# Performance work log

Hardware: AMD Instinct MI355X
Metric: run time of the kernel (lower is better)

## Reference

```python
import jax, jax.numpy as jnp
import numpy as np
import math

N_NODES = 100000
N_GRAPHS = 8
EDGES_PER_GRAPH = 200000
F = 128
RATIO = 0.8


def setup_inputs() -> dict:
    key = jax.random.key(0)
    ks = jax.random.split(key, 24)
    n = N_NODES // N_GRAPHS
    x = jax.random.normal(ks[0], (N_NODES, F), jnp.float32)
    # block-diagonal edges: each graph's edges stay within its node range
    offs = (jnp.arange(N_GRAPHS, dtype=jnp.int32) * n)[:, None]
    src = jax.random.randint(ks[1], (N_GRAPHS, EDGES_PER_GRAPH), 0, n, jnp.int32) + offs
    dst = jax.random.randint(ks[2], (N_GRAPHS, EDGES_PER_GRAPH), 0, n, jnp.int32) + offs
    edge_index = jnp.stack([src.reshape(-1), dst.reshape(-1)])

    def lin(k, fi, fo):
        return jax.random.normal(k, (fo, fi), jnp.float32) / np.sqrt(fi).astype(np.float32)

    inp = dict(x=x, edge_index=edge_index)
    for i, k0 in zip((1, 2, 3), (3, 8, 13)):
        inp[f"W{i}_lin"] = lin(ks[k0], F, F)
        inp[f"b{i}_lin"] = jnp.zeros((F,), jnp.float32)
        inp[f"W{i}_upd"] = lin(ks[k0 + 1], 2 * F, F)   # no bias in update_lin
        inp[f"wp{i}"] = jax.random.normal(ks[k0 + 2], (F,), jnp.float32) / np.float32(np.sqrt(F))
    inp["Wl1"] = lin(ks[18], 2 * F, F); inp["bl1"] = jnp.zeros((F,), jnp.float32)
    inp["Wl2"] = lin(ks[19], F, 64);    inp["bl2"] = jnp.zeros((64,), jnp.float32)
    inp["Wl3"] = lin(ks[20], 64, 1);    inp["bl3"] = jnp.zeros((1,), jnp.float32)
    inp["num_graphs"] = N_GRAPHS
    return inp


def sage_conv(x, edges, W_lin, b_lin, W_upd):
    """Custom SAGEConv: add self loops, msg = relu(lin(x_j)), scatter-max,
    update = relu(update_lin(cat([aggr, x]))). Dummy node at index M absorbs
    edges to/from dropped nodes (never fed back to real nodes)."""
    M = x.shape[0]
    x_ext = jnp.concatenate([x, jnp.zeros((1, x.shape[1]), x.dtype)], 0)  # [M+1, F]
    loops = jnp.arange(M + 1, dtype=edges.dtype)
    src = jnp.concatenate([edges[0], loops])
    dst = jnp.concatenate([edges[1], loops])
    msg = jax.nn.relu(x_ext[src] @ W_lin.T + b_lin)            # gather + linear + relu  [E+M+1, F]
    aggr = jax.ops.segment_max(msg, dst, num_segments=M + 1)   # scatter-max (self loops -> no empty seg)
    out = jax.nn.relu(jnp.concatenate([aggr, x_ext], -1) @ W_upd.T)
    return out[:M]


def topk_pool(x, edges, w, B):
    """TopKPooling(ratio=0.8): score = x.w/||w||, keep top-k per graph,
    x' = x[perm] * tanh(score[perm]); edges remapped, dropped -> dummy Mn."""
    M = x.shape[0]
    n = M // B
    k = int(math.ceil(RATIO * n))
    Mn = B * k
    s = (x @ w) / jnp.linalg.norm(w)
    vals, idx = jax.lax.top_k(s.reshape(B, n), k)              # [B, k]
    gidx = (idx + (jnp.arange(B, dtype=idx.dtype) * n)[:, None]).reshape(-1)
    x_new = x[gidx] * jnp.tanh(vals).reshape(-1)[:, None]
    newpos = jnp.full((M + 1,), Mn, dtype=edges.dtype).at[gidx].set(
        jnp.arange(Mn, dtype=edges.dtype))
    e = newpos[edges]
    invalid = (e[0] == Mn) | (e[1] == Mn)
    e = jnp.where(invalid[None, :], Mn, e)                     # route dropped edges to dummy
    return x_new, e


def readout(x, B):
    xb = x.reshape(B, -1, x.shape[1])                          # graphs are equal-sized
    return jnp.concatenate([xb.max(1), xb.mean(1)], -1)        # gmp || gap  [B, 2F]


def reference(x, edge_index, W1_lin, b1_lin, W1_upd, wp1, W2_lin, b2_lin, W2_upd, wp2,
              W3_lin, b3_lin, W3_upd, wp3, Wl1, bl1, Wl2, bl2, Wl3, bl3, num_graphs):
    B = num_graphs
    h = jax.nn.relu(sage_conv(x, edge_index, W1_lin, b1_lin, W1_upd))
    h, e = topk_pool(h, edge_index, wp1, B); x1 = readout(h, B)
    h = jax.nn.relu(sage_conv(h, e, W2_lin, b2_lin, W2_upd))
    h, e = topk_pool(h, e, wp2, B);          x2 = readout(h, B)
    h = jax.nn.relu(sage_conv(h, e, W3_lin, b3_lin, W3_upd))
    h, e = topk_pool(h, e, wp3, B);          x3 = readout(h, B)
    z = x1 + x2 + x3
    z = jax.nn.relu(z @ Wl1.T + bl1)
    z = jax.nn.relu(z @ Wl2.T + bl2)
    # dropout is identity in eval mode
    return jax.nn.sigmoid(z @ Wl3.T + bl3)[:, 0]
```

## Files before the change

kernel.cpp:

```cpp
#include <hip/hip_runtime.h>
#include <math.h>


typedef unsigned int uint;
typedef unsigned long long ull;

typedef _Float16 h8v __attribute__((ext_vector_type(8)));
typedef _Float16 h4v __attribute__((ext_vector_type(4)));
typedef _Float16 h2v __attribute__((ext_vector_type(2)));
typedef float v4f __attribute__((ext_vector_type(4)));

struct hl16 { _Float16 hi, lo; };

__device__ __forceinline__ float4 ld4(const float* p) { return *reinterpret_cast<const float4*>(p); }
__device__ __forceinline__ float2 ld2(const float* p) { return *reinterpret_cast<const float2*>(p); }

__device__ __forceinline__ uint mono32(float f) {
    uint b = __float_as_uint(f);
    return b ^ ((uint)((int)b >> 31) | 0x80000000u);
}

__device__ __forceinline__ hl16 split16(float x) {
    hl16 r;
    r.hi = (_Float16)x;
    r.lo = (_Float16)(x - (float)r.hi);
    return r;
}

__device__ __forceinline__ h8v hmax8(h8v a, h8v b) {
    return __builtin_elementwise_max(a, b);
}

template<int K, bool A0Z, bool OUT16>
__global__ __launch_bounds__(256, 2)
void mfma_gemm(const _Float16* __restrict__ A0hi, const _Float16* __restrict__ A0lo,
               const _Float16* __restrict__ A1hi, const _Float16* __restrict__ A1lo,
               const _Float16* __restrict__ Whi, const _Float16* __restrict__ Wlo,
               const float* __restrict__ bias, void* __restrict__ outv, int M)
{
    constexpr int LDT = 40;
    __shared__ __align__(16) _Float16 As[128 * LDT];
    __shared__ __align__(16) _Float16 Ws[128 * LDT];
    const int tid = threadIdx.x;
    const int lane = tid & 63;
    const int wv = tid >> 6;
    const int wr = (wv >> 1) * 64;
    const int wc = (wv & 1) * 64;
    const int quad = lane >> 4;
    const int l16 = lane & 15;
    const int row0 = blockIdx.x * 128;

    const int sr0 = tid >> 2;
    const int sr1 = sr0 + 64;
    const int sq = (tid & 3) * 8;
    const bool ok0 = (row0 + sr0) < M;
    const bool ok1 = (row0 + sr1) < M;

    v4f acc[4][4];
#pragma unroll
    for (int i = 0; i < 4; ++i)
#pragma unroll
        for (int j = 0; j < 4; ++j) acc[i][j] = (v4f){0.f, 0.f, 0.f, 0.f};

    constexpr int CPS = K / 32;
    constexpr int NS2 = A0Z ? (K - 128) / 32 : CPS;
    constexpr int NC = 2 * CPS + NS2;
    float4 pa0, pa1, pw0, pw1;
    const float4 f4z = make_float4(0.f, 0.f, 0.f, 0.f);

#define GLOAD(C) do { \
        int kc_, kk_; const _Float16 *Wp_, *Ap_; bool lo_ = (C) >= 2 * CPS; \
        if ((C) < CPS)          { kc_ = (C) * 32;          Wp_ = Whi; } \
        else if ((C) < 2 * CPS) { kc_ = ((C) - CPS) * 32;  Wp_ = Wlo; } \
        else                    { kc_ = ((C) - 2 * CPS) * 32 + (A0Z ? 128 : 0); Wp_ = Whi; } \
        if (K == 256 && kc_ >= 128) { Ap_ = lo_ ? A1lo : A1hi; kk_ = kc_ - 128; } \
        else                        { Ap_ = lo_ ? A0lo : A0hi; kk_ = kc_; } \
        pa0 = ok0 ? ld4((const float*)(Ap_ + (size_t)(row0 + sr0) * 128 + kk_ + sq)) : f4z; \
        pa1 = ok1 ? ld4((const float*)(Ap_ + (size_t)(row0 + sr1) * 128 + kk_ + sq)) : f4z; \
        pw0 = ld4((const float*)(Wp_ + (size_t)sr0 * K + kc_ + sq)); \
        pw1 = ld4((const float*)(Wp_ + (size_t)sr1 * K + kc_ + sq)); \
    } while (0)

#define SSTORE() do { \
        *reinterpret_cast<float4*>(&As[sr0 * LDT + sq]) = pa0; \
        *reinterpret_cast<float4*>(&As[sr1 * LDT + sq]) = pa1; \
        *reinterpret_cast<float4*>(&Ws[sr0 * LDT + sq]) = pw0; \
        *reinterpret_cast<float4*>(&Ws[sr1 * LDT + sq]) = pw1; \
    } while (0)

    GLOAD(0);
#pragma unroll
    for (int c = 0; c < NC; ++c) {
        SSTORE();
        __syncthreads();
        if (c + 1 < NC) GLOAD(c + 1);
        h8v af[4], bf[4];
#pragma unroll
        for (int rt = 0; rt < 4; ++rt)
            af[rt] = *reinterpret_cast<const h8v*>(&As[(wr + rt * 16 + l16) * LDT + quad * 8]);
#pragma unroll
        for (int ct = 0; ct < 4; ++ct)
            bf[ct] = *reinterpret_cast<const h8v*>(&Ws[(wc + ct * 16 + l16) * LDT + quad * 8]);
#pragma unroll
        for (int rt = 0; rt < 4; ++rt)
#pragma unroll
            for (int ct = 0; ct < 4; ++ct)
                acc[rt][ct] = __builtin_amdgcn_mfma_f32_16x16x32_f16(
                    af[rt], bf[ct], acc[rt][ct], 0, 0, 0);
        if (c + 1 < NC) __syncthreads();
    }
#undef GLOAD
#undef SSTORE

    float bv[4];
#pragma unroll
    for (int ct = 0; ct < 4; ++ct)
        bv[ct] = bias ? bias[wc + ct * 16 + l16] : 0.f;
#pragma unroll
    for (int rt = 0; rt < 4; ++rt) {
        int rb = row0 + wr + rt * 16 + quad * 4;
#pragma unroll
        for (int r = 0; r < 4; ++r) {
            int row = rb + r;
            if (row < M) {
                if (OUT16) {
                    _Float16* op = (_Float16*)outv + (size_t)row * 128;
#pragma unroll
                    for (int ct = 0; ct < 4; ++ct)
                        op[wc + ct * 16 + l16] =
                            (_Float16)fmaxf(acc[rt][ct][r] + bv[ct], 0.f);
                } else {
                    float* op = (float*)outv + (size_t)row * 128;
#pragma unroll
                    for (int ct = 0; ct < 4; ++ct)
                        op[wc + ct * 16 + l16] = fmaxf(acc[rt][ct][r] + bv[ct], 0.f);
                }
            }
        }
    }
}

__global__ void prep_weights(const float* __restrict__ s0, const float* __restrict__ s1,
                             const float* __restrict__ s2, const float* __restrict__ s3,
                             const float* __restrict__ s4, const float* __restrict__ s5,
                             _Float16* __restrict__ WLhi, _Float16* __restrict__ WLlo,
                             _Float16* __restrict__ WUhi, _Float16* __restrict__ WUlo)
{
    int i = blockIdx.x * 256 + threadIdx.x;
    if (i < 3 * 16384) {
        int m = i / 16384, o = i - m * 16384;
        const float* s = (m == 0) ? s0 : (m == 1) ? s2 : s4;
        hl16 r = split16(s[o]);
        WLhi[i] = r.hi; WLlo[i] = r.lo;
    } else if (i < 3 * 16384 + 3 * 32768) {
        int j = i - 3 * 16384;
        int m = j / 32768, o = j - m * 32768;
        const float* s = (m == 0) ? s1 : (m == 1) ? s3 : s5;
        hl16 r = split16(s[o]);
        WUhi[j] = r.hi; WUlo[j] = r.lo;
    }
}

__global__ void convert_x(const float* __restrict__ x, _Float16* __restrict__ hi,
                          _Float16* __restrict__ lo, int total4)
{
    int i = blockIdx.x * 256 + threadIdx.x;
    if (i >= total4) return;
    float4 v = ld4(x + (size_t)i * 4);
    h4v H, L;
    hl16 r0 = split16(v.x); H[0] = r0.hi; L[0] = r0.lo;
    hl16 r1 = split16(v.y); H[1] = r1.hi; L[1] = r1.lo;
    hl16 r2 = split16(v.z); H[2] = r2.hi; L[2] = r2.lo;
    hl16 r3 = split16(v.w); H[3] = r3.hi; L[3] = r3.lo;
    *reinterpret_cast<h4v*>(hi + (size_t)i * 4) = H;
    *reinterpret_cast<h4v*>(lo + (size_t)i * 4) = L;
}

#define SC_T 16
#define SC_CH (256 * SC_T)
__global__ __launch_bounds__(256)
void bucket_scatter(const int* __restrict__ esrc, const int* __restrict__ edst,
                    int* __restrict__ bcur, uint* __restrict__ bkt,
                    int Eg, int n, int NB, int CAP)
{
    __shared__ int lcnt[64];
    __shared__ int lbase[64];
    int g = blockIdx.x & 7;
    int c = blockIdx.x >> 3;
    int t = threadIdx.x;
    if (t < 64) lcnt[t] = 0;
    __syncthreads();
    int e0i = c * SC_CH;
    uint pk[SC_T];
    int bkid[SC_T];
    int loc[SC_T];
#pragma unroll
    for (int j = 0; j < SC_T; ++j) {
        int o = e0i + j * 256 + t;
        bkid[j] = -1;
        if (o < Eg) {
            int i = g * Eg + o;
            int dl = edst[i] - g * n;
            int b = dl >> 8;
            pk[j] = ((uint)dl << 17) | (uint)esrc[i];
            bkid[j] = b;
            loc[j] = atomicAdd(&lcnt[b], 1);
        }
    }
    __syncthreads();
    if (t < NB && lcnt[t] > 0)
        lbase[t] = atomicAdd(&bcur[g * NB + t], lcnt[t]);
    __syncthreads();
#pragma unroll
    for (int j = 0; j < SC_T; ++j) {
        if (bkid[j] >= 0) {
            int b = bkid[j];
            int slot = lbase[b] + loc[j];
            if (slot < CAP)
                bkt[(size_t)(g * NB + b) * CAP + slot] = pk[j];
        }
    }
}

__global__ __launch_bounds__(256)
void csr_build(const int* __restrict__ bcur, const uint* __restrict__ bkt,
               int* __restrict__ rowptr, int* __restrict__ csr,
               int Eg, int n, int NB, int CAP)
{
    __shared__ uint eLDS[5120];
    __shared__ int outLDS[5120];
    __shared__ int hist[256];
    __shared__ int curL[256];
    __shared__ int wpart[4];
    __shared__ int sh_base, sh_cnt;
    int g = blockIdx.x & 7;
    int b = blockIdx.x >> 3;
    int t = threadIdx.x;
    if (t < 64) {
        int c = 0;
        if (t < NB) { c = bcur[g * NB + t]; c = c > CAP ? CAP : c; }
        int s = c;
#pragma unroll
        for (int off = 1; off < 64; off <<= 1) {
            int x = __shfl_up(s, off);
            if (t >= off) s += x;
        }
        if (t == b) { sh_base = g * Eg + s - c; sh_cnt = c; }
    }
    hist[t] = 0;
    __syncthreads();
    const int base = sh_base;
    const int cnt = sh_cnt;
    const uint* bk = bkt + (size_t)(g * NB + b) * CAP;
    for (int i = t; i < cnt; i += 256) {
        uint e = bk[i];
        eLDS[i] = e;
        atomicAdd(&hist[(e >> 17) & 255], 1);
    }
    __syncthreads();
    int lane = t & 63, w = t >> 6;
    int v = hist[t], s = v;
#pragma unroll
    for (int off = 1; off < 64; off <<= 1) {
        int x = __shfl_up(s, off);
        if (lane >= off) s += x;
    }
    if (lane == 63) wpart[w] = s;
    __syncthreads();
    if (t == 0) {
        int a = 0;
#pragma unroll
        for (int i = 0; i < 4; ++i) { int x = wpart[i]; wpart[i] = a; a += x; }
    }
    __syncthreads();
    int incl = s + wpart[w];
    curL[t] = incl - v;
    int nodeg = b * 256 + t;
    if (nodeg < n) rowptr[(size_t)g * n + nodeg] = base + incl;
    __syncthreads();
    for (int i = t; i < cnt; i += 256) {
        uint e = eLDS[i];
        int pos = atomicAdd(&curL[(e >> 17) & 255], 1);
        outLDS[pos] = (int)(e & 0x1FFFFu);
    }
    __syncthreads();
    for (int i = t; i < cnt; i += 256) csr[base + i] = outLDS[i];
}

__global__ void compose_kernel(int* __restrict__ cur, const int* __restrict__ newpos,
                               const int* __restrict__ oldidx, const int* __restrict__ org_in,
                               int* __restrict__ org_out, int N, int Mnew, int Mout, int first)
{
    int i = blockIdx.x * 256 + threadIdx.x;
    if (i < N) {
        int c = first ? i : cur[i];
        int r = -1;
        if (c >= 0) {
            int np = newpos[c];
            if (np < Mout) r = np;
        }
        cur[i] = r;
    }
    if (i < Mnew)
        org_out[i] = first ? oldidx[i] : org_in[oldidx[i]];
}

__global__ __launch_bounds__(256)
void aggr_max(const _Float16* __restrict__ Yh, const int* __restrict__ rowptr,
              const int* __restrict__ csr, const int* __restrict__ cur,
              const int* __restrict__ org, _Float16* __restrict__ Ghi, int k)
{
    int b = blockIdx.x;
    int g = b & 7;
    int chunk = b >> 3;
    int wid = __builtin_amdgcn_readfirstlane((int)(threadIdx.x >> 6));
    int lane = threadIdx.x & 63;
    int node = g * k + chunk * 4 + wid;
    int sub = lane >> 4;
    int fo = (lane & 15) * 8;
    int v0 = org ? org[node] : node;
    int beg, end;
    if (v0) {
        int2 be = *reinterpret_cast<const int2*>(rowptr + v0 - 1);
        beg = be.x; end = be.y;
    } else {
        beg = 0; end = rowptr[0];
    }
    h8v acc = *reinterpret_cast<const h8v*>(Yh + (size_t)node * 128 + fo);
    int p = beg;
    for (; p + 8 <= end; p += 8) {
        int s0 = csr[p + sub];
        int s1 = csr[p + 4 + sub];
        if (cur) {
            int c0 = cur[s0]; s0 = (c0 >= 0) ? c0 : node;
            int c1 = cur[s1]; s1 = (c1 >= 0) ? c1 : node;
        }
        h8v w0 = *reinterpret_cast<const h8v*>(Yh + (size_t)s0 * 128 + fo);
        h8v w1 = *reinterpret_cast<const h8v*>(Yh + (size_t)s1 * 128 + fo);
        acc = hmax8(acc, w0);
        acc = hmax8(acc, w1);
    }
    for (; p + 4 <= end; p += 4) {
        int s = csr[p + sub];
        if (cur) { int c2 = cur[s]; s = (c2 >= 0) ? c2 : node; }
        h8v v = *reinterpret_cast<const h8v*>(Yh + (size_t)s * 128 + fo);
        acc = hmax8(acc, v);
    }
    if (p < end) {
        int idx = p + sub;
        int s = node;
        if (idx < end) {
            s = csr[idx];
            if (cur) { int c2 = cur[s]; s = (c2 >= 0) ? c2 : node; }
        }
        h8v v = *reinterpret_cast<const h8v*>(Yh + (size_t)s * 128 + fo);
        acc = hmax8(acc, v);
    }
#pragma unroll
    for (int off = 16; off <= 32; off <<= 1) {
        int4 u = *reinterpret_cast<int4*>(&acc);
        int4 o;
        o.x = __shfl_xor(u.x, off);
        o.y = __shfl_xor(u.y, off);
        o.z = __shfl_xor(u.z, off);
        o.w = __shfl_xor(u.w, off);
        acc = hmax8(acc, *reinterpret_cast<h8v*>(&o));
    }
    if (sub == 0)
        *reinterpret_cast<h8v*>(Ghi + (size_t)node * 128 + fo) = acc;
}

__global__ __launch_bounds__(256)
void score_kernel(const float* __restrict__ H, const float* __restrict__ wp,
                  float* __restrict__ s, int M)
{
    int wid = threadIdx.x >> 6;
    int lane = threadIdx.x & 63;
    int node = blockIdx.x * 4 + wid;
    if (node >= M) return;
    float2 h = ld2(H + (size_t)node * 128 + lane * 2);
    float2 w = ld2(wp + lane * 2);
    float d = h.x * w.x + h.y * w.y;
    float nn = w.x * w.x + w.y * w.y;
    for (int off = 1; off < 64; off <<= 1) {
        d += __shfl_xor(d, off);
        nn += __shfl_xor(nn, off);
    }
    if (lane == 0) s[node] = d / sqrtf(nn);
}

__global__ __launch_bounds__(1024)
void topk_kernel(const float* __restrict__ s, int* __restrict__ newpos,
                 int* __restrict__ oldidx, int n, int k, int Mout)
{
    __shared__ uint keys[12512];
    __shared__ __align__(16) int hist[256];
    __shared__ uint sh_prefix;
    __shared__ int sh_need;
    __shared__ int sh_cnt;
    __shared__ int sh_eq;
    __shared__ int eqlist[2048];
    int g = blockIdx.x;
    int t = threadIdx.x;
    const float* sg = s + (size_t)g * n;
    for (int i = t; i < n; i += 1024) keys[i] = mono32(sg[i]);
    if (t == 0) { sh_prefix = 0u; sh_need = k; sh_cnt = 0; sh_eq = 0; }
    __syncthreads();
    for (int pass = 3; pass >= 0; --pass) {
        int shift = pass * 8;
        if (t < 256) hist[t] = 0;
        __syncthreads();
        uint pref = sh_prefix;
        uint maskhi = (pass == 3) ? 0u : (0xFFFFFFFFu << (shift + 8));
        for (int i = t; i < n; i += 1024) {
            uint m = keys[i];
            if ((m & maskhi) == pref)
                atomicAdd(&hist[(m >> shift) & 255], 1);
        }
        __syncthreads();
        if (t < 64) {
            int need = sh_need;
            int4 h = *reinterpret_cast<const int4*>(&hist[t * 4]);
            int s3 = h.w;
            int s2 = h.z + s3;
            int s1 = h.y + s2;
            int s0 = h.x + s1;
            int tot = s0;
            int suf = tot;
#pragma unroll
            for (int off = 1; off < 64; off <<= 1) {
                int v = __shfl_down(suf, off);
                if (t + off < 64) suf += v;
            }
            int above = suf - tot;
            int v0 = s0 + above, v1 = s1 + above, v2 = s2 + above, v3 = s3 + above;
            int n3 = (t == 63) ? 0 : above;
            int bsel = -1, nextv = 0;
            if      (v3 >= need && n3 < need) { bsel = 4 * t + 3; nextv = n3; }
            else if (v2 >= need && v3 < need) { bsel = 4 * t + 2; nextv = v3; }
            else if (v1 >= need && v2 < need) { bsel = 4 * t + 1; nextv = v2; }
            else if (v0 >= need && v1 < need) { bsel = 4 * t + 0; nextv = v1; }
            if (bsel >= 0) {
                sh_prefix = pref | ((uint)bsel << shift);
                sh_need = need - nextv;
            }
        }
        __syncthreads();
    }
    uint pivot = sh_prefix;
    int take_eq = sh_need;
    for (int i = t; i < n; i += 1024) {
        uint m = keys[i];
        if (m > pivot) {
            int pos = g * k + atomicAdd(&sh_cnt, 1);
            newpos[g * n + i] = pos;
            oldidx[pos] = g * n + i;
        } else {
            if (m == pivot) {
                int e = atomicAdd(&sh_eq, 1);
                if (e < 2048) eqlist[e] = i;
            }
            newpos[g * n + i] = Mout;
        }
    }
    __syncthreads();
    int ec = sh_eq < 2048 ? sh_eq : 2048;
    for (int e = t; e < ec; e += 1024) {
        int idx = eqlist[e];
        int rank = 0;
        for (int j = 0; j < ec; ++j) rank += (eqlist[j] < idx);
        if (rank < take_eq) {
            int pos = g * k + atomicAdd(&sh_cnt, 1);
            newpos[g * n + idx] = pos;
            oldidx[pos] = g * n + idx;
        }
    }
}

__global__ __launch_bounds__(256)
void permute_kernel(const float* __restrict__ H, const float* __restrict__ s,
                    const int* __restrict__ oldidx, _Float16* __restrict__ Xhi,
                    _Float16* __restrict__ Xlo, int Mout)
{
    int wid = __builtin_amdgcn_readfirstlane((int)(threadIdx.x >> 6));
    int lane = threadIdx.x & 63;
    int pos = blockIdx.x * 4 + wid;
    if (pos >= Mout) return;
    int old = oldidx[pos];
    float scv = tanhf(s[old]);
    float2 v = ld2(H + (size_t)old * 128 + lane * 2);
    v.x *= scv; v.y *= scv;
    h2v H2, L2;
    hl16 r0 = split16(v.x); H2[0] = r0.hi; L2[0] = r0.lo;
    hl16 r1 = split16(v.y); H2[1] = r1.hi; L2[1] = r1.lo;
    *reinterpret_cast<h2v*>(Xhi + (size_t)pos * 128 + lane * 2) = H2;
    *reinterpret_cast<h2v*>(Xlo + (size_t)pos * 128 + lane * 2) = L2;
}

#define RO_NC 32
__global__ __launch_bounds__(256)
void readout_kernel(const _Float16* __restrict__ Xhi, const _Float16* __restrict__ Xlo,
                    uint* __restrict__ zmax, float* __restrict__ zsum, int k)
{
    __shared__ float rmx[4][128];
    __shared__ float rsm[4][128];
    int g = blockIdx.x & 7;
    int c = blockIdx.x >> 3;
    int t = threadIdx.x;
    int wv = t >> 6;
    int lane = t & 63;
    int slot = t >> 4;
    int fo = (lane & 15) * 8;
    int chunk = (k + RO_NC - 1) / RO_NC;
    int r0 = c * chunk;
    int r1 = r0 + chunk; if (r1 > k) r1 = k;
    float mx[8], sm[8];
#pragma unroll
    for (int j = 0; j < 8; ++j) { mx[j] = -INFINITY; sm[j] = 0.f; }
    for (int r = r0 + slot; r < r1; r += 16) {
        size_t base = (size_t)(g * k + r) * 128 + fo;
        h8v hi = *reinterpret_cast<const h8v*>(Xhi + base);
        h8v lo = *reinterpret_cast<const h8v*>(Xlo + base);
#pragma unroll
        for (int j = 0; j < 8; ++j) {
            float v = (float)hi[j] + (float)lo[j];
            mx[j] = fmaxf(mx[j], v);
            sm[j] += v;
        }
    }
#pragma unroll
    for (int off = 16; off <= 32; off <<= 1) {
#pragma unroll
        for (int j = 0; j < 8; ++j) {
            mx[j] = fmaxf(mx[j], __shfl_xor(mx[j], off));
            sm[j] += __shfl_xor(sm[j], off);
        }
    }
    if ((lane >> 4) == 0) {
#pragma unroll
        for (int j = 0; j < 8; ++j) {
            rmx[wv][fo + j] = mx[j];
            rsm[wv][fo + j] = sm[j];
        }
    }
    __syncthreads();
    if (t < 128) {
        float m = fmaxf(fmaxf(rmx[0][t], rmx[1][t]), fmaxf(rmx[2][t], rmx[3][t]));
        float s = (rsm[0][t] + rsm[1][t]) + (rsm[2][t] + rsm[3][t]);
        atomicMax(&zmax[g * 128 + t], mono32(m));
        atomicAdd(&zsum[g * 128 + t], s);
    }
}

__global__ __launch_bounds__(256)
void zs_prep(const uint* __restrict__ zmaxu, const float* __restrict__ zsum,
             int k1, int k2, int k3, float* __restrict__ zsg)
{
    int i = blockIdx.x * 256 + threadIdx.x;
    int g = i >> 8, f = i & 255;
    float kk[3] = {(float)k1, (float)k2, (float)k3};
    float a = 0.f;
    if (f < 128) {
        for (int l = 0; l < 3; ++l) {
            uint u = zmaxu[l * 1024 + g * 128 + f];
            a += (u & 0x80000000u) ? __uint_as_float(u ^ 0x80000000u)
                                   : __uint_as_float(~u);
        }
    } else {
        int ff = f - 128;
        for (int l = 0; l < 3; ++l)
            a += zsum[l * 1024 + g * 128 + ff] / kk[l];
    }
    zsg[i] = a;
}

__global__ __launch_bounds__(256)
void mlp1(const float* __restrict__ zsg, const float* __restrict__ Wl1,
          const float* __restrict__ bl1, float* __restrict__ h1g)
{
    int wv = threadIdx.x >> 6, lane = threadIdx.x & 63;
    int o = blockIdx.x * 4 + wv;
    int g = o >> 7, f = o & 127;
    float4 w = ld4(Wl1 + (size_t)f * 256 + lane * 4);
    float4 z = ld4(zsg + (size_t)g * 256 + lane * 4);
    float a = w.x * z.x + w.y * z.y + w.z * z.z + w.w * z.w;
#pragma unroll
    for (int off = 1; off < 64; off <<= 1) a += __shfl_xor(a, off);
    if (lane == 0) h1g[o] = fmaxf(a + bl1[f], 0.f);
}

__global__ __launch_bounds__(256)
void mlp2(const float* __restrict__ h1g, const float* __restrict__ Wl2,
          const float* __restrict__ bl2, float* __restrict__ h2g)
{
    int wv = threadIdx.x >> 6, lane = threadIdx.x & 63;
    int o = blockIdx.x * 4 + wv;
    int g = o >> 6, f = o & 63;
    float2 w = ld2(Wl2 + (size_t)f * 128 + lane * 2);
    float2 h = ld2(h1g + (size_t)g * 128 + lane * 2);
    float a = w.x * h.x + w.y * h.y;
#pragma unroll
    for (int off = 1; off < 64; off <<= 1) a += __shfl_xor(a, off);
    if (lane == 0) h2g[o] = fmaxf(a + bl2[f], 0.f);
}

__global__ __launch_bounds__(512)
void mlp3(const float* __restrict__ h2g, const float* __restrict__ Wl3,
          const float* __restrict__ bl3, float* __restrict__ out)
{
    int g = threadIdx.x >> 6, lane = threadIdx.x & 63;
    float a = h2g[g * 64 + lane] * Wl3[lane];
#pragma unroll
    for (int off = 1; off < 64; off <<= 1) a += __shfl_xor(a, off);
    if (lane == 0) out[g] = 1.f / (1.f + expf(-(a + bl3[0])));
}

extern "C" void kernel_launch(void* const* d_in, const int* in_sizes, int n_in,
                              void* d_out, int out_size, void* d_ws, size_t ws_size,
                              hipStream_t stream)
{
    const float* x0 = (const float*)d_in[0];
    const int* e0 = (const int*)d_in[1];
    const int E = in_sizes[1] / 2;
    const int N = in_sizes[0] / 128;
    const int B = 8;
    const int Eg = E / B;

    char* p = (char*)d_ws;
    auto carve = [&](size_t bytes) -> char* {
        char* r = p;
        p += (bytes + 255) & ~(size_t)255;
        return r;
    };
    _Float16* B0h = (_Float16*)carve((size_t)100000 * 128 * 2);
    _Float16* B0l = (_Float16*)carve((size_t)100000 * 128 * 2);
    _Float16* B1h = (_Float16*)carve((size_t)100000 * 128 * 2);
    _Float16* B1l = (_Float16*)carve((size_t)100000 * 128 * 2);
    _Float16* Yh  = (_Float16*)carve((size_t)100000 * 128 * 2);
    float* Y      = (float*)carve((size_t)100000 * 128 * 4);
    int*   csr    = (int*)carve((size_t)E * 4);
    int*   rowptr = (int*)carve(100000 * 4);
    float* sc     = (float*)carve(100000 * 4);
    int*   newpos = (int*)carve(100000 * 4);
    int*   oldidx = (int*)carve(80000 * 4);
    int*   cur    = (int*)carve(100000 * 4);
    int*   orgA   = (int*)carve(80000 * 4);
    int*   orgB   = (int*)carve(80000 * 4);
    int*   bcur   = (int*)carve(8 * 64 * 4);
    _Float16* WLhi = (_Float16*)carve(3 * 16384 * 2);
    _Float16* WLlo = (_Float16*)carve(3 * 16384 * 2);
    _Float16* WUhi = (_Float16*)carve(3 * 32768 * 2);
    _Float16* WUlo = (_Float16*)carve(3 * 32768 * 2);
    uint*  zmaxu  = (uint*)carve(3 * 1024 * 4);
    float* zsum   = (float*)carve(3 * 1024 * 4);
    float* zsg    = (float*)carve(8 * 256 * 4);
    float* h1g    = (float*)carve(8 * 128 * 4);
    float* h2g    = (float*)carve(8 * 64 * 4);

    (void)hipMemsetAsync(zmaxu, 0, 6 * 1024 * 4, stream);
    (void)hipMemsetAsync(bcur, 0, 8 * 64 * 4, stream);
    prep_weights<<<(3 * 16384 + 3 * 32768 + 255) / 256, 256, 0, stream>>>(
        (const float*)d_in[2], (const float*)d_in[4], (const float*)d_in[6],
        (const float*)d_in[8], (const float*)d_in[10], (const float*)d_in[12],
        WLhi, WLlo, WUhi, WUlo);
    convert_x<<<(N * 32 + 255) / 256, 256, 0, stream>>>(x0, B0h, B0l, N * 32);

    int n1 = N / B;
    int NB = (n1 + 255) >> 8;
    const int CAP = 5120;
    uint* bkt = (uint*)Y;
    int nchunk = (Eg + SC_CH - 1) / SC_CH;
    bucket_scatter<<<8 * nchunk, 256, 0, stream>>>(e0, e0 + E, bcur, bkt, Eg, n1, NB, CAP);
    csr_build<<<NB * 8, 256, 0, stream>>>(bcur, bkt, rowptr, csr, Eg, n1, NB, CAP);

    int M = N;
    for (int l = 0; l < 3; ++l) {
        int n = M / B;
        int k = (int)ceil(0.8 * (double)n);
        int Mout = B * k;
        const float* blin = (const float*)d_in[3 + 4 * l];
        const float* wp   = (const float*)d_in[5 + 4 * l];
        _Float16* XIh = (l & 1) ? B1h : B0h;
        _Float16* XIl = (l & 1) ? B1l : B0l;
        _Float16* XOh = (l & 1) ? B0h : B1h;
        _Float16* XOl = (l & 1) ? B0l : B1l;
        const int* curp = (l == 0) ? nullptr : cur;
        const int* orgp = (l == 0) ? nullptr : ((l == 1) ? orgA : orgB);
        int gb = (M + 127) / 128;

        mfma_gemm<128, false, true><<<gb, 256, 0, stream>>>(XIh, XIl, nullptr, nullptr,
            WLhi + l * 16384, WLlo + l * 16384, blin, Yh, M);
        aggr_max<<<M / 4, 256, 0, stream>>>(Yh, rowptr, csr, curp, orgp, XOh, n);
        mfma_gemm<256, true, false><<<gb, 256, 0, stream>>>(XOh, nullptr, XIh, XIl,
            WUhi + l * 32768, WUlo + l * 32768, nullptr, Y, M);

        score_kernel<<<(M + 3) / 4, 256, 0, stream>>>(Y, wp, sc, M);
        topk_kernel<<<B, 1024, 0, stream>>>(sc, newpos, oldidx, n, k, Mout);
        permute_kernel<<<(Mout + 3) / 4, 256, 0, stream>>>(Y, sc, oldidx, XOh, XOl, Mout);

        readout_kernel<<<8 * RO_NC, 256, 0, stream>>>(XOh, XOl,
            zmaxu + l * 1024, zsum + l * 1024, k);

        if (l < 2) {
            compose_kernel<<<(N + 255) / 256, 256, 0, stream>>>(
                cur, newpos, oldidx, (l == 0) ? nullptr : orgA,
                (l == 0) ? orgA : orgB, N, Mout, Mout, (l == 0) ? 1 : 0);
        }
        M = Mout;
    }

    int kk1 = 10000, kk2 = 8000, kk3 = 6400;
    zs_prep<<<8, 256, 0, stream>>>(zmaxu, zsum, kk1, kk2, kk3, zsg);
    mlp1<<<256, 256, 0, stream>>>(zsg, (const float*)d_in[14], (const float*)d_in[15], h1g);
    mlp2<<<128, 256, 0, stream>>>(h1g, (const float*)d_in[16], (const float*)d_in[17], h2g);
    mlp3<<<1, 512, 0, stream>>>(h2g, (const float*)d_in[18], (const float*)d_in[19],
                                (float*)d_out);
}
```

Baseline: 595.7 us.

## Fuse hi/lo split-precision passes into a single K loop in MFMA GEMM

The split-fp16 GEMM used to run separate passes over K for A_hi*W_hi, A_hi*W_lo and A_lo*W_hi, each reloading tiles. Now each K chunk loads the hi and lo tiles of both A and W together into four LDS buffers and issues all three MFMA groups per chunk. The number of barriers and loop iterations drops and the A_hi tiles are reused. This doubles LDS use and raises register pressure, and the launch bounds drop the min-2-blocks hint, so occupancy may fall. The null check on the A-lo pointer is now a runtime test inside the loop.

```diff
diff --git a/kernel.cpp b/kernel.cpp
--- a/kernel.cpp
+++ b/kernel.cpp
@@ -32,15 +32,17 @@
 }
 
 template<int K, bool A0Z, bool OUT16>
-__global__ __launch_bounds__(256, 2)
+__global__ __launch_bounds__(256)
 void mfma_gemm(const _Float16* __restrict__ A0hi, const _Float16* __restrict__ A0lo,
                const _Float16* __restrict__ A1hi, const _Float16* __restrict__ A1lo,
                const _Float16* __restrict__ Whi, const _Float16* __restrict__ Wlo,
                const float* __restrict__ bias, void* __restrict__ outv, int M)
 {
     constexpr int LDT = 40;
-    __shared__ __align__(16) _Float16 As[128 * LDT];
-    __shared__ __align__(16) _Float16 Ws[128 * LDT];
+    __shared__ __align__(16) _Float16 Ah[128 * LDT];
+    __shared__ __align__(16) _Float16 Al[128 * LDT];
+    __shared__ __align__(16) _Float16 Wh[128 * LDT];
+    __shared__ __align__(16) _Float16 Wl[128 * LDT];
     const int tid = threadIdx.x;
     const int lane = tid & 63;
     const int wv = tid >> 6;
@@ -62,55 +64,87 @@
 #pragma unroll
         for (int j = 0; j < 4; ++j) acc[i][j] = (v4f){0.f, 0.f, 0.f, 0.f};
 
-    constexpr int CPS = K / 32;
-    constexpr int NS2 = A0Z ? (K - 128) / 32 : CPS;
-    constexpr int NC = 2 * CPS + NS2;
-    float4 pa0, pa1, pw0, pw1;
+    constexpr int NCH = K / 32;
+    float4 ph0, ph1, pl0, pl1, qh0, qh1, ql0, ql1;
     const float4 f4z = make_float4(0.f, 0.f, 0.f, 0.f);
 
+#define CHUNK_LO(C) ((((K == 256) && ((C) >= 4)) ? A1lo : A0lo) != nullptr)
+
 #define GLOAD(C) do { \
-        int kc_, kk_; const _Float16 *Wp_, *Ap_; bool lo_ = (C) >= 2 * CPS; \
-        if ((C) < CPS)          { kc_ = (C) * 32;          Wp_ = Whi; } \
-        else if ((C) < 2 * CPS) { kc_ = ((C) - CPS) * 32;  Wp_ = Wlo; } \
-        else                    { kc_ = ((C) - 2 * CPS) * 32 + (A0Z ? 128 : 0); Wp_ = Whi; } \
-        if (K == 256 && kc_ >= 128) { Ap_ = lo_ ? A1lo : A1hi; kk_ = kc_ - 128; } \
-        else                        { Ap_ = lo_ ? A0lo : A0hi; kk_ = kc_; } \
-        pa0 = ok0 ? ld4((const float*)(Ap_ + (size_t)(row0 + sr0) * 128 + kk_ + sq)) : f4z; \
-        pa1 = ok1 ? ld4((const float*)(Ap_ + (size_t)(row0 + sr1) * 128 + kk_ + sq)) : f4z; \
-        pw0 = ld4((const float*)(Wp_ + (size_t)sr0 * K + kc_ + sq)); \
-        pw1 = ld4((const float*)(Wp_ + (size_t)sr1 * K + kc_ + sq)); \
+        int kc_ = (C) * 32, kk_; const _Float16 *ah_, *al_; \
+        if (K == 256 && kc_ >= 128) { ah_ = A1hi; al_ = A1lo; kk_ = kc_ - 128; } \
+        else                        { ah_ = A0hi; al_ = A0lo; kk_ = kc_; } \
+        ph0 = ok0 ? ld4((const float*)(ah_ + (size_t)(row0 + sr0) * 128 + kk_ + sq)) : f4z; \
+        ph1 = ok1 ? ld4((const float*)(ah_ + (size_t)(row0 + sr1) * 128 + kk_ + sq)) : f4z; \
+        if (al_) { \
+            pl0 = ok0 ? ld4((const float*)(al_ + (size_t)(row0 + sr0) * 128 + kk_ + sq)) : f4z; \
+            pl1 = ok1 ? ld4((const float*)(al_ + (size_t)(row0 + sr1) * 128 + kk_ + sq)) : f4z; \
+        } \
+        qh0 = ld4((const float*)(Whi + (size_t)sr0 * K + kc_ + sq)); \
+        qh1 = ld4((const float*)(Whi + (size_t)sr1 * K + kc_ + sq)); \
+        ql0 = ld4((const float*)(Wlo + (size_t)sr0 * K + kc_ + sq)); \
+        ql1 = ld4((const float*)(Wlo + (size_t)sr1 * K + kc_ + sq)); \
     } while (0)
 
-#define SSTORE() do { \
-        *reinterpret_cast<float4*>(&As[sr0 * LDT + sq]) = pa0; \
-        *reinterpret_cast<float4*>(&As[sr1 * LDT + sq]) = pa1; \
-        *reinterpret_cast<float4*>(&Ws[sr0 * LDT + sq]) = pw0; \
-        *reinterpret_cast<float4*>(&Ws[sr1 * LDT + sq]) = pw1; \
+#define SSTORE(C) do { \
+        *reinterpret_cast<float4*>(&Ah[sr0 * LDT + sq]) = ph0; \
+        *reinterpret_cast<float4*>(&Ah[sr1 * LDT + sq]) = ph1; \
+        if (CHUNK_LO(C)) { \
+            *reinterpret_cast<float4*>(&Al[sr0 * LDT + sq]) = pl0; \
+            *reinterpret_cast<float4*>(&Al[sr1 * LDT + sq]) = pl1; \
+        } \
+        *reinterpret_cast<float4*>(&Wh[sr0 * LDT + sq]) = qh0; \
+        *reinterpret_cast<float4*>(&Wh[sr1 * LDT + sq]) = qh1; \
+        *reinterpret_cast<float4*>(&Wl[sr0 * LDT + sq]) = ql0; \
+        *reinterpret_cast<float4*>(&Wl[sr1 * LDT + sq]) = ql1; \
     } while (0)
 
     GLOAD(0);
 #pragma unroll
-    for (int c = 0; c < NC; ++c) {
-        SSTORE();
+    for (int c = 0; c < NCH; ++c) {
+        SSTORE(c);
         __syncthreads();
-        if (c + 1 < NC) GLOAD(c + 1);
-        h8v af[4], bf[4];
+        const bool hl = CHUNK_LO(c);
+        if (c + 1 < NCH) GLOAD(c + 1);
+        h8v afh[4], afl[4], bfh[4], bfl[4];
 #pragma unroll
         for (int rt = 0; rt < 4; ++rt)
-            af[rt] = *reinterpret_cast<const h8v*>(&As[(wr + rt * 16 + l16) * LDT + quad * 8]);
-#pragma unroll
-        for (int ct = 0; ct < 4; ++ct)
-            bf[ct] = *reinterpret_cast<const h8v*>(&Ws[(wc + ct * 16 + l16) * LDT + quad * 8]);
+            afh[rt] = *reinterpret_cast<const h8v*>(&Ah[(wr + rt * 16 + l16) * LDT + quad * 8]);
+#pragma unroll
+        for (int ct = 0; ct < 4; ++ct) {
+            bfh[ct] = *reinterpret_cast<const h8v*>(&Wh[(wc + ct * 16 + l16) * LDT + quad * 8]);
+            bfl[ct] = *reinterpret_cast<const h8v*>(&Wl[(wc + ct * 16 + l16) * LDT + quad * 8]);
+        }
+        if (hl) {
+#pragma unroll
+            for (int rt = 0; rt < 4; ++rt)
+                afl[rt] = *reinterpret_cast<const h8v*>(&Al[(wr + rt * 16 + l16) * LDT + quad * 8]);
+        }
 #pragma unroll
         for (int rt = 0; rt < 4; ++rt)
 #pragma unroll
             for (int ct = 0; ct < 4; ++ct)
                 acc[rt][ct] = __builtin_amdgcn_mfma_f32_16x16x32_f16(
-                    af[rt], bf[ct], acc[rt][ct], 0, 0, 0);
-        if (c + 1 < NC) __syncthreads();
+                    afh[rt], bfh[ct], acc[rt][ct], 0, 0, 0);
+#pragma unroll
+        for (int rt = 0; rt < 4; ++rt)
+#pragma unroll
+            for (int ct = 0; ct < 4; ++ct)
+                acc[rt][ct] = __builtin_amdgcn_mfma_f32_16x16x32_f16(
+                    afh[rt], bfl[ct], acc[rt][ct], 0, 0, 0);
+        if (hl) {
+#pragma unroll
+            for (int rt = 0; rt < 4; ++rt)
+#pragma unroll
+                for (int ct = 0; ct < 4; ++ct)
+                    acc[rt][ct] = __builtin_amdgcn_mfma_f32_16x16x32_f16(
+                        afl[rt], bfh[ct], acc[rt][ct], 0, 0, 0);
+        }
+        if (c + 1 < NCH) __syncthreads();
     }
 #undef GLOAD
 #undef SSTORE
+#undef CHUNK_LO
 
     float bv[4];
 #pragma unroll
```

After: 583.6 us (median of 2 runs). 1.02x faster.
